# Kernel optimization log

Hardware: AMD Instinct MI355X
Metric: run time of the kernel (lower is better)

Reference implementation:

```python
import jax, jax.numpy as jnp
import numpy as np

N_HEADS = 16


def setup_inputs() -> dict:
    key = jax.random.key(0)
    k1, k2, k3 = jax.random.split(key, 3)
    B, S, D = 2, 2048, 1024
    x = jax.random.normal(k1, (B, S, D), dtype=jnp.float32)
    # causal mask: 1 = keep, 0 = masked (module does masked_fill(mask == 0, -inf))
    mask = jnp.broadcast_to(jnp.tril(jnp.ones((S, S), dtype=jnp.int32)), (B, S, S))
    # torch Linear(bias=False) weights, stored transposed so y = x @ W
    w_qkv = jax.random.normal(k2, (D, 3 * D), dtype=jnp.float32) * (1.0 / np.sqrt(D))
    w_out = jax.random.normal(k3, (D, D), dtype=jnp.float32) * (1.0 / np.sqrt(D))
    return {"x": x, "mask": mask, "w_qkv": w_qkv, "w_out": w_out}


def reference(x, mask, w_qkv, w_out):
    B, S, D = x.shape
    H = N_HEADS
    dh = D // H
    scale = 1.0 / np.sqrt(dh)

    qkv = x @ w_qkv                                   # [B,S,3D]
    qkv = qkv.reshape(B, S, 3, H, dh)
    qkv = jnp.transpose(qkv, (2, 0, 3, 1, 4))         # [3,B,H,S,dh]
    q, k, v = qkv[0], qkv[1], qkv[2]

    scores = jnp.einsum("bhqd,bhkd->bhqk", q, k) * scale   # [B,H,S,S]
    scores = jnp.where(mask[:, None, :, :] == 0, -jnp.inf, scores)
    attn = jax.nn.softmax(scores, axis=-1)            # dropout = identity (eval)

    out = jnp.einsum("bhqk,bhkd->bhqd", attn, v)      # [B,H,S,dh]
    out = jnp.transpose(out, (0, 2, 1, 3)).reshape(B, S, D)
    return out @ w_out
```

## Files before the change

kernel.cpp:

```cpp
#include <hip/hip_runtime.h>

typedef unsigned short u16;
typedef unsigned int u32;
typedef u16 u16x8 __attribute__((ext_vector_type(8)));
typedef u16 u16x4 __attribute__((ext_vector_type(4)));
typedef u32 u32x4 __attribute__((ext_vector_type(4)));
typedef __bf16 bf16x8 __attribute__((ext_vector_type(8)));
typedef float f32x4 __attribute__((ext_vector_type(4)));
typedef float f32x16 __attribute__((ext_vector_type(16)));


static __device__ __forceinline__ u16 bf16_rn(float f) {
    union { float f; u32 u; } a; a.f = f;
    u32 u = a.u;
    return (u16)((u + 0x7FFFu + ((u >> 16) & 1u)) >> 16);
}

static __device__ __forceinline__ bf16x8 as_bf(u16x8 v) {
    return __builtin_bit_cast(bf16x8, v);
}

static __device__ __forceinline__ u32 cvt_pk_bf16(float lo, float hi) {
    u32 r;
    asm("v_cvt_pk_bf16_f32 %0, %1, %2" : "=v"(r) : "v"(lo), "v"(hi));
    return r;
}

static __device__ __forceinline__ void glds16(const u16* g, u16* lds) {
    __builtin_amdgcn_global_load_lds(
        (const __attribute__((address_space(1))) void*)g,
        (__attribute__((address_space(3))) void*)lds, 16, 0, 0);
}


__global__ void k_cvt(const float* __restrict__ src, u16* __restrict__ dst, int n8) {
    int i = blockIdx.x * blockDim.x + threadIdx.x;
    if (i >= n8) return;
    const float4* s = (const float4*)src + (size_t)i * 2;
    float4 a = s[0], b = s[1];
    u16x8 v;
    v[0] = bf16_rn(a.x); v[1] = bf16_rn(a.y); v[2] = bf16_rn(a.z); v[3] = bf16_rn(a.w);
    v[4] = bf16_rn(b.x); v[5] = bf16_rn(b.y); v[6] = bf16_rn(b.z); v[7] = bf16_rn(b.w);
    *(u16x8*)(dst + (size_t)i * 8) = v;
}


__global__ void k_tr_cvt(const float* __restrict__ src, u16* __restrict__ dst,
                         int R, int C) {
    __shared__ float t[32][33];
    const int bx = blockIdx.x * 32, by = blockIdx.y * 32;
    const int tx = threadIdx.x, ty = threadIdx.y;
#pragma unroll
    for (int j = 0; j < 32; j += 8)
        t[ty + j][tx] = src[(size_t)(by + ty + j) * C + bx + tx];
    __syncthreads();
#pragma unroll
    for (int j = 0; j < 32; j += 8)
        dst[(size_t)(bx + ty + j) * R + by + tx] = bf16_rn(t[tx][ty + j]);
}


template <int MODE>
__launch_bounds__(256, 2)
__global__ void k_gemm(const u16* __restrict__ A, const u16* __restrict__ Bt,
                       void* __restrict__ outp, int M, int N, int K) {
    __shared__ __align__(16) u16 As[2][128 * 32];
    __shared__ __align__(16) u16 Bs[2][128 * 32];
    const int tid = threadIdx.x;
    const int l = tid & 63, wv = tid >> 6;
    const int wr = wv >> 1, wc = wv & 1;
    const int l15 = l & 15, lg = l >> 4;
    const int m0 = blockIdx.y * 128, n0 = blockIdx.x * 128;
    const int NT = K >> 5;

    const f32x4 fzero = {0.f, 0.f, 0.f, 0.f};
    f32x4 acc[4][4];
#pragma unroll
    for (int m = 0; m < 4; m++)
#pragma unroll
        for (int n = 0; n < 4; n++) acc[m][n] = fzero;

    const int grow0 = wv * 32 + (l >> 2);
    const int gcol = (l & 3) * 8;

    auto stage = [&](int buf, int kt) {
        const size_t ko = (size_t)kt * 32 + gcol;
        glds16(A  + (size_t)(m0 + grow0) * K + ko,      &As[buf][wv * 1024]);
        glds16(A  + (size_t)(m0 + grow0 + 16) * K + ko, &As[buf][wv * 1024 + 512]);
        glds16(Bt + (size_t)(n0 + grow0) * K + ko,      &Bs[buf][wv * 1024]);
        glds16(Bt + (size_t)(n0 + grow0 + 16) * K + ko, &Bs[buf][wv * 1024 + 512]);
    };

    stage(0, 0);
    int cur = 0;
    for (int kt = 0; kt < NT; ++kt) {
        if (kt + 1 < NT) {
            stage(cur ^ 1, kt + 1);
            asm volatile("s_waitcnt vmcnt(4)" ::: "memory");
        } else {
            asm volatile("s_waitcnt vmcnt(0)" ::: "memory");
        }
        __builtin_amdgcn_s_barrier();
        u16x8 af[4], bfv[4];
#pragma unroll
        for (int m = 0; m < 4; m++)
            af[m] = *(const u16x8*)(&As[cur][(wr * 64 + m * 16 + l15) * 32 + lg * 8]);
#pragma unroll
        for (int n = 0; n < 4; n++)
            bfv[n] = *(const u16x8*)(&Bs[cur][(wc * 64 + n * 16 + l15) * 32 + lg * 8]);
#pragma unroll
        for (int m = 0; m < 4; m++)
#pragma unroll
            for (int n = 0; n < 4; n++)
                acc[m][n] = __builtin_amdgcn_mfma_f32_16x16x32_bf16(
                    as_bf(af[m]), as_bf(bfv[n]), acc[m][n], 0, 0, 0);
        __builtin_amdgcn_s_barrier();
        cur ^= 1;
    }

    if (MODE == 0) {
        u16* qkv = (u16*)outp;
#pragma unroll
        for (int m = 0; m < 4; m++) {
            const int rb = m0 + wr * 64 + m * 16 + lg * 4;
#pragma unroll
            for (int n = 0; n < 4; n++) {
                const int c = n0 + wc * 64 + n * 16;
                const int t = c >> 10, h = (c >> 6) & 15, d0 = (c & 63) + l15;
                const float scl = (t == 0) ? 0.18033688011112042f : 1.0f;
#pragma unroll
                for (int i = 0; i < 4; i++) {
                    const int r = rb + i;
                    const int b = r >> 11, s = r & 2047;
                    qkv[((((size_t)t * 2 + b) * 16 + h) * 2048 + s) * 64 + d0] =
                        bf16_rn(acc[m][n][i] * scl);
                }
            }
        }
    } else {
        float* O = (float*)outp;
#pragma unroll
        for (int m = 0; m < 4; m++) {
            const int rb = m0 + wr * 64 + m * 16 + lg * 4;
#pragma unroll
            for (int n = 0; n < 4; n++) {
                const int c = n0 + wc * 64 + n * 16 + l15;
#pragma unroll
                for (int i = 0; i < 4; i++)
                    O[(size_t)(rb + i) * N + c] = acc[m][n][i];
            }
        }
    }
}


__launch_bounds__(256, 3)
__global__ void k_attn(const u16* __restrict__ qkv, u16* __restrict__ ab) {
    __shared__ __align__(16) char arena[4][9216];
    __shared__ float MLs[4][64];
    const int tid = threadIdx.x, l = tid & 63, wv = tid >> 6;
    const int q = l & 31, h = l >> 5;
    const int bid = blockIdx.x;
    const int bh = bid & 31;
    const int pp = bid >> 5;
    const int b = bh >> 4, hd = bh & 15;
    const size_t plane = (size_t)2048 * 64;
    const u16* Qg = qkv + ((size_t)(0 + b) * 16 + hd) * plane;
    const u16* Kg = qkv + ((size_t)(2 + b) * 16 + hd) * plane;
    const u16* Vg = qkv + ((size_t)(4 + b) * 16 + hd) * plane;
    u16* VT = (u16*)arena[wv];

    const int g = l & 7, qd = l >> 3;
    const u16* Kbase = Kg + (size_t)q * 64 + 8 * h;
    const u16* Vbase = Vg + (size_t)(8 * qd) * 64 + 8 * g;
    const int Fq0 = 8 * (q >> 3) + ((q & 7) ^ ((q >> 3) & 7));
    const int d1 = q + 32;
    const int Fq1 = 8 * (d1 >> 3) + ((d1 & 7) ^ ((d1 >> 3) & 7));
    const u16* vr0 = VT + Fq0 * 72 + 8 * h;
    const u16* vr1 = VT + Fq1 * 72 + 8 * h;
    const float FIXM = 12.0f;

    for (int ph = 0; ph < 2; ++ph) {
        const int qt = ph ? 63 - pp : pp;
        const int q0 = qt * 32, qg = q0 + q;
        const int n64 = (qt >> 1) + 1;

        u16x8 qf[4];
#pragma unroll
        for (int s = 0; s < 4; ++s)
            qf[s] = *(const u16x8*)(Qg + (size_t)(q0 + q) * 64 + s * 16 + 8 * h);

        f32x16 oacc0 = 0, oacc1 = 0;
        float l_run = 0.f;

        u16x8 vK[8];
        if (wv < n64) {
#pragma unroll
            for (int s = 0; s < 4; ++s) {
                vK[s]     = *(const u16x8*)(Kbase + (size_t)(wv * 64) * 64 + s * 16);
                vK[4 + s] = *(const u16x8*)(Kbase + (size_t)(wv * 64 + 32) * 64 + s * 16);
            }
        }

        for (int t = wv; t < n64; t += 4) {
            const int kv0 = t * 64;
            u16x8 vV[8];
#pragma unroll
            for (int j = 0; j < 8; ++j)
                vV[j] = *(const u16x8*)(Vbase + (size_t)(kv0 + j) * 64);
            f32x16 sa = 0, sb = 0;
            __builtin_amdgcn_s_setprio(1);
#pragma unroll
            for (int s = 0; s < 4; ++s)
                sa = __builtin_amdgcn_mfma_f32_32x32x16_bf16(as_bf(vK[s]), as_bf(qf[s]), sa, 0, 0, 0);
#pragma unroll
            for (int s = 0; s < 4; ++s)
                sb = __builtin_amdgcn_mfma_f32_32x32x16_bf16(as_bf(vK[4 + s]), as_bf(qf[s]), sb, 0, 0, 0);
            __builtin_amdgcn_s_setprio(0);
#pragma unroll
            for (int j = 0; j < 8; ++j) {
                u16x8 col;
#pragma unroll
                for (int r = 0; r < 8; ++r) col[r] = vV[r][j];
                *(u16x8*)(VT + (size_t)(8 * g + (j ^ g)) * 72 + 8 * qd) = col;
            }
            if (t + 4 < n64) {
#pragma unroll
                for (int s = 0; s < 4; ++s) {
                    vK[s]     = *(const u16x8*)(Kbase + (size_t)((t + 4) * 64) * 64 + s * 16);
                    vK[4 + s] = *(const u16x8*)(Kbase + (size_t)((t + 4) * 64 + 32) * 64 + s * 16);
                }
            }
            if (t == n64 - 1) {
#pragma unroll
                for (int r = 0; r < 16; ++r) {
                    const int kg = kv0 + (r & 3) + 8 * (r >> 2) + 4 * h;
                    if (kg > qg) sa[r] = -__builtin_inff();
                    if (kg + 32 > qg) sb[r] = -__builtin_inff();
                }
            }
#pragma unroll
            for (int r = 0; r < 16; ++r) sa[r] = exp2f(sa[r] - FIXM);
#pragma unroll
            for (int r = 0; r < 16; ++r) sb[r] = exp2f(sb[r] - FIXM);
            float ts[8];
#pragma unroll
            for (int i = 0; i < 8; ++i)
                ts[i] = (sa[i] + sa[i + 8]) + (sb[i] + sb[i + 8]);
#pragma unroll
            for (int i = 0; i < 4; ++i) ts[i] += ts[i + 4];
            l_run += (ts[0] + ts[2]) + (ts[1] + ts[3]);
            u32 pk[16];
#pragma unroll
            for (int i = 0; i < 8; ++i) pk[i]     = cvt_pk_bf16(sa[2 * i], sa[2 * i + 1]);
#pragma unroll
            for (int i = 0; i < 8; ++i) pk[8 + i] = cvt_pk_bf16(sb[2 * i], sb[2 * i + 1]);
#pragma unroll
            for (int ks = 0; ks < 4; ++ks) {
                const int base = (ks >> 1) * 8 + 4 * (ks & 1);
                const u32 o0 = pk[base], o1 = pk[base + 1], o2 = pk[base + 2], o3 = pk[base + 3];
                const u32 sd0 = h ? o0 : o2, sd1 = h ? o1 : o3;
                const u32 r0 = (u32)__shfl_xor((int)sd0, 32);
                const u32 r1 = (u32)__shfl_xor((int)sd1, 32);
                const u32 w0 = h ? r0 : o0, w1 = h ? r1 : o1;
                const u32 w2 = h ? o2 : r0, w3 = h ? o3 : r1;
                const u16x8 pb = __builtin_bit_cast(u16x8, (u32x4){w0, w1, w2, w3});
                const u16x8 va0 = *(const u16x8*)(vr0 + ks * 16);
                const u16x8 va1 = *(const u16x8*)(vr1 + ks * 16);
                __builtin_amdgcn_s_setprio(1);
                oacc0 = __builtin_amdgcn_mfma_f32_32x32x16_bf16(as_bf(va0), as_bf(pb), oacc0, 0, 0, 0);
                oacc1 = __builtin_amdgcn_mfma_f32_32x32x16_bf16(as_bf(va1), as_bf(pb), oacc1, 0, 0, 0);
                __builtin_amdgcn_s_setprio(0);
            }
        }
        asm volatile("" ::: "memory");
        float* Op = (float*)arena[wv];
#pragma unroll
        for (int r = 0; r < 16; ++r) {
            const int dr = (r & 3) + 8 * (r >> 2) + 4 * h;
            Op[q * 64 + ((dr + 2 * q) & 63)]      = oacc0[r];
            Op[q * 64 + ((dr + 32 + 2 * q) & 63)] = oacc1[r];
        }
        MLs[wv][l] = l_run;
        __syncthreads();
        const int tq = tid >> 3, dblk = (tid & 7) * 8;
        float L = 0.f;
#pragma unroll
        for (int w = 0; w < 4; ++w) L += MLs[w][tq] + MLs[w][32 + tq];
        const float inv = 1.f / L;
        u16x8 outv;
#pragma unroll
        for (int j = 0; j < 8; ++j) {
            const int d = dblk + j;
            float acc = 0.f;
#pragma unroll
            for (int w = 0; w < 4; ++w)
                acc += ((const float*)arena[w])[tq * 64 + ((d + 2 * tq) & 63)];
            outv[j] = bf16_rn(acc * inv);
        }
        *(u16x8*)(ab + (size_t)(b * 2048 + q0 + tq) * 1024 + hd * 64 + dblk) = outv;
        __syncthreads();
    }
}


extern "C" void kernel_launch(void* const* d_in, const int* in_sizes, int n_in,
                              void* d_out, int out_size, void* d_ws, size_t ws_size,
                              hipStream_t stream) {
    const float* x     = (const float*)d_in[0];
    const float* w_qkv = (const float*)d_in[2];
    const float* w_out = (const float*)d_in[3];
    float* out = (float*)d_out;
    u16* ws = (u16*)d_ws;

    u16* xb    = ws;
    u16* wqkvT = ws + 4194304;
    u16* woutT = ws + 7340032;
    u16* qkvb  = ws + 8388608;
    u16* abuf  = ws;

    k_cvt<<<2048, 256, 0, stream>>>(x, xb, 524288);
    k_tr_cvt<<<dim3(96, 32), dim3(32, 8), 0, stream>>>(w_qkv, wqkvT, 1024, 3072);
    k_tr_cvt<<<dim3(32, 32), dim3(32, 8), 0, stream>>>(w_out, woutT, 1024, 1024);
    k_gemm<0><<<dim3(24, 32), 256, 0, stream>>>(xb, wqkvT, qkvb, 4096, 3072, 1024);
    k_attn<<<1024, 256, 0, stream>>>(qkvb, abuf);
    k_gemm<1><<<dim3(8, 32), 256, 0, stream>>>(abuf, woutT, out, 4096, 1024, 1024);
}
```

Before: 134.4 us.

## Store V transposed from QKV projection and load attention V operands directly

The QKV projection epilogue now writes the V plane transposed (d-major, s contiguous), so the attention kernel can load MFMA A-operands for P·V straight from global memory. This drops the per-tile register transpose and LDS staging of V, and shrinks shared memory to just the output reduction buffer. The next-K prefetch is moved after the softmax conversion. The cost is strided scalar 2-byte stores in the GEMM epilogue for the V part, which scatter writes across rows of 2048 elements.

```diff
diff --git a/kernel.cpp b/kernel.cpp
--- a/kernel.cpp
+++ b/kernel.cpp
@@ -132,8 +132,12 @@
                 for (int i = 0; i < 4; i++) {
                     const int r = rb + i;
                     const int b = r >> 11, s = r & 2047;
-                    qkv[((((size_t)t * 2 + b) * 16 + h) * 2048 + s) * 64 + d0] =
-                        bf16_rn(acc[m][n][i] * scl);
+                    const size_t pbase = (((size_t)t * 2 + b) * 16 + h) * 131072;
+                    const u16 val = bf16_rn(acc[m][n][i] * scl);
+                    if (t == 2)
+                        qkv[pbase + (size_t)d0 * 2048 + s] = val;
+                    else
+                        qkv[pbase + (size_t)s * 64 + d0] = val;
                 }
             }
         }
@@ -156,7 +160,7 @@
 
 __launch_bounds__(256, 3)
 __global__ void k_attn(const u16* __restrict__ qkv, u16* __restrict__ ab) {
-    __shared__ __align__(16) char arena[4][9216];
+    __shared__ float Oprt[4][2048];
     __shared__ float MLs[4][64];
     const int tid = threadIdx.x, l = tid & 63, wv = tid >> 6;
     const int q = l & 31, h = l >> 5;
@@ -167,17 +171,10 @@
     const size_t plane = (size_t)2048 * 64;
     const u16* Qg = qkv + ((size_t)(0 + b) * 16 + hd) * plane;
     const u16* Kg = qkv + ((size_t)(2 + b) * 16 + hd) * plane;
-    const u16* Vg = qkv + ((size_t)(4 + b) * 16 + hd) * plane;
-    u16* VT = (u16*)arena[wv];
-
-    const int g = l & 7, qd = l >> 3;
-    const u16* Kbase = Kg + (size_t)q * 64 + 8 * h;
-    const u16* Vbase = Vg + (size_t)(8 * qd) * 64 + 8 * g;
-    const int Fq0 = 8 * (q >> 3) + ((q & 7) ^ ((q >> 3) & 7));
-    const int d1 = q + 32;
-    const int Fq1 = 8 * (d1 >> 3) + ((d1 & 7) ^ ((d1 >> 3) & 7));
-    const u16* vr0 = VT + Fq0 * 72 + 8 * h;
-    const u16* vr1 = VT + Fq1 * 72 + 8 * h;
+    const u16* Vt = qkv + ((size_t)(4 + b) * 16 + hd) * plane;
+
+    const u16* Kbase  = Kg + (size_t)q * 64 + 8 * h;
+    const u16* VTbase = Vt + (size_t)q * 2048 + 8 * h;
     const float FIXM = 12.0f;
 
     for (int ph = 0; ph < 2; ++ph) {
@@ -204,10 +201,12 @@
 
         for (int t = wv; t < n64; t += 4) {
             const int kv0 = t * 64;
-            u16x8 vV[8];
-#pragma unroll
-            for (int j = 0; j < 8; ++j)
-                vV[j] = *(const u16x8*)(Vbase + (size_t)(kv0 + j) * 64);
+            u16x8 vA0[4], vA1[4];
+#pragma unroll
+            for (int ks = 0; ks < 4; ++ks) {
+                vA0[ks] = *(const u16x8*)(VTbase + kv0 + ks * 16);
+                vA1[ks] = *(const u16x8*)(VTbase + 65536 + kv0 + ks * 16);
+            }
             f32x16 sa = 0, sb = 0;
             __builtin_amdgcn_s_setprio(1);
 #pragma unroll
@@ -217,20 +216,6 @@
             for (int s = 0; s < 4; ++s)
                 sb = __builtin_amdgcn_mfma_f32_32x32x16_bf16(as_bf(vK[4 + s]), as_bf(qf[s]), sb, 0, 0, 0);
             __builtin_amdgcn_s_setprio(0);
-#pragma unroll
-            for (int j = 0; j < 8; ++j) {
-                u16x8 col;
-#pragma unroll
-                for (int r = 0; r < 8; ++r) col[r] = vV[r][j];
-                *(u16x8*)(VT + (size_t)(8 * g + (j ^ g)) * 72 + 8 * qd) = col;
-            }
-            if (t + 4 < n64) {
-#pragma unroll
-                for (int s = 0; s < 4; ++s) {
-                    vK[s]     = *(const u16x8*)(Kbase + (size_t)((t + 4) * 64) * 64 + s * 16);
-                    vK[4 + s] = *(const u16x8*)(Kbase + (size_t)((t + 4) * 64 + 32) * 64 + s * 16);
-                }
-            }
             if (t == n64 - 1) {
 #pragma unroll
                 for (int r = 0; r < 16; ++r) {
@@ -255,6 +240,13 @@
             for (int i = 0; i < 8; ++i) pk[i]     = cvt_pk_bf16(sa[2 * i], sa[2 * i + 1]);
 #pragma unroll
             for (int i = 0; i < 8; ++i) pk[8 + i] = cvt_pk_bf16(sb[2 * i], sb[2 * i + 1]);
+            if (t + 4 < n64) {
+#pragma unroll
+                for (int s = 0; s < 4; ++s) {
+                    vK[s]     = *(const u16x8*)(Kbase + (size_t)((t + 4) * 64) * 64 + s * 16);
+                    vK[4 + s] = *(const u16x8*)(Kbase + (size_t)((t + 4) * 64 + 32) * 64 + s * 16);
+                }
+            }
 #pragma unroll
             for (int ks = 0; ks < 4; ++ks) {
                 const int base = (ks >> 1) * 8 + 4 * (ks & 1);
@@ -265,16 +257,13 @@
                 const u32 w0 = h ? r0 : o0, w1 = h ? r1 : o1;
                 const u32 w2 = h ? o2 : r0, w3 = h ? o3 : r1;
                 const u16x8 pb = __builtin_bit_cast(u16x8, (u32x4){w0, w1, w2, w3});
-                const u16x8 va0 = *(const u16x8*)(vr0 + ks * 16);
-                const u16x8 va1 = *(const u16x8*)(vr1 + ks * 16);
                 __builtin_amdgcn_s_setprio(1);
-                oacc0 = __builtin_amdgcn_mfma_f32_32x32x16_bf16(as_bf(va0), as_bf(pb), oacc0, 0, 0, 0);
-                oacc1 = __builtin_amdgcn_mfma_f32_32x32x16_bf16(as_bf(va1), as_bf(pb), oacc1, 0, 0, 0);
+                oacc0 = __builtin_amdgcn_mfma_f32_32x32x16_bf16(as_bf(vA0[ks]), as_bf(pb), oacc0, 0, 0, 0);
+                oacc1 = __builtin_amdgcn_mfma_f32_32x32x16_bf16(as_bf(vA1[ks]), as_bf(pb), oacc1, 0, 0, 0);
                 __builtin_amdgcn_s_setprio(0);
             }
         }
-        asm volatile("" ::: "memory");
-        float* Op = (float*)arena[wv];
+        float* Op = Oprt[wv];
 #pragma unroll
         for (int r = 0; r < 16; ++r) {
             const int dr = (r & 3) + 8 * (r >> 2) + 4 * h;
@@ -295,7 +284,7 @@
             float acc = 0.f;
 #pragma unroll
             for (int w = 0; w < 4; ++w)
-                acc += ((const float*)arena[w])[tq * 64 + ((d + 2 * tq) & 63)];
+                acc += Oprt[w][tq * 64 + ((d + 2 * tq) & 63)];
             outv[j] = bf16_rn(acc * inv);
         }
         *(u16x8*)(ab + (size_t)(b * 2048 + q0 + tq) * 1024 + hd * 64 + dblk) = outv;
```

Result: slower. 164.3 us (+22.2%).
